# Kernel optimization log

Measured on AMD Instinct MI355X. Metric: run time of the kernel, lower is better.

## Reference

```python
import jax, jax.numpy as jnp
import numpy as np

B, N, F_ATOM, F_PATH = 32, 64, 82, 102
H, DK, HIDDEN, DEPTH = 8, 80, 256, 3
EPS = 1e-20


def setup_inputs() -> dict:
    key = jax.random.key(0)
    ks = jax.random.split(key, 12)
    s = lambda shape: 0.05
    inp = {
        "atom_input": jax.random.normal(ks[0], (B, N, F_ATOM), jnp.float32),
        "path_input": jax.random.normal(ks[1], (B, N, N, F_PATH), jnp.float32),
        # binary neighbor mask (path_mask); mask_neigh=True -> attn_mask = path_mask
        "path_mask": (jax.random.uniform(ks[2], (B, N, N)) < 0.25).astype(jnp.float32),
        "W_atom_i": jax.random.normal(ks[3], (F_ATOM, H * DK), jnp.float32) * 0.05,
        "W_attn_h": jax.random.normal(ks[4], (2 * DK + F_PATH, DK), jnp.float32) * 0.05,
        "b_attn_h": jax.random.normal(ks[5], (DK,), jnp.float32) * 0.05,
        "W_attn_o": jax.random.normal(ks[6], (DK, 1), jnp.float32) * 0.05,
        "b_attn_o": jax.random.normal(ks[7], (1,), jnp.float32) * 0.05,
        "W_msg_h": jax.random.normal(ks[8], (2 * DK + F_PATH, DK), jnp.float32) * 0.05,
        "b_msg_h": jax.random.normal(ks[9], (DK,), jnp.float32) * 0.05,
        "W_atom_o": jax.random.normal(ks[10], (F_ATOM + H * DK, HIDDEN), jnp.float32) * 0.05,
        "b_atom_o": jax.random.normal(ks[11], (HIDDEN,), jnp.float32) * 0.05,
    }
    return inp


def _forward(atom_input, path_input, path_mask,
             W_atom_i, W_attn_h, b_attn_h, W_attn_o, b_attn_o,
             W_msg_h, b_msg_h, W_atom_o, b_atom_o):
    # project atoms and split heads: [B,N,H*DK] -> [H*B, N, DK]
    atom_h0 = (atom_input @ W_atom_i).reshape(B, N, H, DK)
    atom_h0 = jnp.transpose(atom_h0, (2, 0, 1, 3)).reshape(H * B, N, DK)

    # tile path features / mask across heads (torch .repeat(n_heads,1,1,1))
    path_t = jnp.tile(path_input, (H, 1, 1, 1))          # [H*B, N, N, F_PATH]
    mask_t = jnp.tile(path_mask, (H, 1, 1))[..., None]    # [H*B, N, N, 1]

    atom_h = atom_h0
    for _ in range(DEPTH - 1):
        # pairwise expand + concat: [H*B, N, N, 2*DK + F_PATH]
        a1 = jnp.broadcast_to(atom_h[:, :, None, :], (H * B, N, N, DK))
        a2 = jnp.broadcast_to(atom_h[:, None, :, :], (H * B, N, N, DK))
        attn_input = jnp.concatenate([a1, a2, path_t], axis=3)

        # score MLP -> masked softmax over dim 2 (neighbors j)
        scores = jax.nn.leaky_relu(attn_input @ W_attn_h + b_attn_h, 0.2)
        scores = (scores @ W_attn_o + b_attn_o) * mask_t      # [H*B,N,N,1]
        max_s = jnp.max(scores, axis=2, keepdims=True)
        exp_s = jnp.exp(scores - max_s) * mask_t
        probs = exp_s / (jnp.sum(exp_s, axis=2, keepdims=True) + EPS) * mask_t

        # weighted message sum + residual
        msg = jnp.sum(probs * attn_input, axis=2)             # [H*B, N, 2DK+F_PATH]
        atom_h = jax.nn.relu(msg @ W_msg_h + b_msg_h + atom_h0)

    # merge heads back: [H*B,N,DK] -> [B,N,H*DK] -> [B*N, H*DK]
    atom_h = atom_h.reshape(H, B, N, DK)
    atom_h = jnp.transpose(atom_h, (1, 2, 0, 3)).reshape(B * N, H * DK)

    atom_2d = atom_input.reshape(B * N, F_ATOM)
    out = jnp.concatenate([atom_2d, atom_h], axis=1)
    return jax.nn.relu(out @ W_atom_o + b_atom_o)             # [B*N, HIDDEN]


def reference(atom_input, path_input, path_mask,
              W_atom_i, W_attn_h, b_attn_h, W_attn_o, b_attn_o,
              W_msg_h, b_msg_h, W_atom_o, b_atom_o):
    return _forward(atom_input, path_input, path_mask,
                    W_atom_i, W_attn_h, b_attn_h, W_attn_o, b_attn_o,
                    W_msg_h, b_msg_h, W_atom_o, b_atom_o)
```

## Files before the change

### kernel.cpp

```cpp
#include <hip/hip_runtime.h>
#include <hip/hip_bf16.h>

typedef __hip_bfloat16 bf16;
typedef _Float16 half2v __attribute__((ext_vector_type(2)));
typedef _Float16 half8  __attribute__((ext_vector_type(8)));
typedef float  float4v __attribute__((ext_vector_type(4)));
typedef unsigned uint4v __attribute__((ext_vector_type(4)));
typedef short  short8 __attribute__((ext_vector_type(8)));
typedef float  f32x4  __attribute__((ext_vector_type(4)));


__device__ inline float bflo(unsigned w) { return __uint_as_float(w << 16); }
__device__ inline float bfhi(unsigned w) { return __uint_as_float(w & 0xFFFF0000u); }
__device__ inline unsigned pack2bf(float x, float y) {
    bf16 a = (bf16)x, c = (bf16)y;
    unsigned short ua = *(unsigned short*)&a, uc = *(unsigned short*)&c;
    return (unsigned)ua | ((unsigned)uc << 16);
}
__device__ inline unsigned pack2h(float x, float y) {
    _Float16 a = (_Float16)x, c = (_Float16)y;
    unsigned short ua = *(unsigned short*)&a, uc = *(unsigned short*)&c;
    return (unsigned)ua | ((unsigned)uc << 16);
}
__device__ inline half2v ash2(unsigned u) { return __builtin_bit_cast(half2v, u); }
__device__ inline unsigned asu2(half2v h) { return __builtin_bit_cast(unsigned, h); }

__device__ inline float fdot2acc(half2v a, half2v b, float s) {
#if __has_builtin(__builtin_amdgcn_fdot2)
    return __builtin_amdgcn_fdot2(a, b, s, false);
#else
    return s + (float)a.x * (float)b.x + (float)a.y * (float)b.y;
#endif
}

__global__ __launch_bounds__(256) void prep_kernel(
    const float* __restrict__ W_atom_i, const float* __restrict__ W_attn_h,
    const float* __restrict__ b_attn_h, const float* __restrict__ W_msg_h,
    const float* __restrict__ W_atom_o,
    bf16* __restrict__ WTg, bf16* __restrict__ WTu, bf16* __restrict__ WTa,
    _Float16* __restrict__ WTo, float* __restrict__ buvam)
{
    int tid0 = blockIdx.x * 256 + threadIdx.x;
    int NT = gridDim.x * 256;
    for (int t = tid0; t < 2 * 80 * 128; t += NT) {
        int z = t / 10240, rem = t - z * 10240;
        int n = rem >> 7, k = rem & 127;
        const float* src = z ? W_msg_h : W_attn_h;
        WTg[t] = (bf16)((k < 102) ? src[(160 + k) * 80 + n] : 0.f);
    }
    for (int t = tid0; t < 4 * 80 * 96; t += NT) {
        int z = t / 7680, rem = t - z * 7680;
        int n = rem / 96, k = rem - n * 96;
        const float* src = (z < 2) ? W_attn_h : W_msg_h;
        WTu[t] = (bf16)((k < 80) ? src[((z & 1) * 80 + k) * 80 + n] : 0.f);
    }
    for (int t = tid0; t < 8 * 80 * 96; t += NT) {
        int h = t / 7680, rem = t - h * 7680;
        int n = rem / 96, k = rem - n * 96;
        WTa[t] = (bf16)((k < 82) ? W_atom_i[k * 640 + h * 80 + n] : 0.f);
    }
    for (int t = tid0; t < 256 * 736; t += NT) {
        int n = t / 736, f = t - n * 736;
        WTo[t] = (_Float16)((f < 722) ? W_atom_o[(size_t)f * 256 + n] : 0.f);
    }
    for (int t = tid0; t < 320; t += NT)
        buvam[t] = (t < 80) ? b_attn_h[t] : 0.f;
}

__global__ __launch_bounds__(320) void atom_proj_mfma(
    const float* __restrict__ atom, const bf16* __restrict__ WTa,
    float* __restrict__ ah0)
{
    __shared__ bf16 Als[64 * 104];
    int t = threadIdx.x;
    int rowBase = blockIdx.x * 64;
    int h = blockIdx.y;
    int wave = t >> 6, lane = t & 63, ln = lane & 15, quad = lane >> 4;

    const short* Wp = (const short*)(WTa + (size_t)h * 80 * 96);
    short8 bfrag[3];
    #pragma unroll
    for (int kc = 0; kc < 3; kc++)
        bfrag[kc] = *(const short8*)(Wp + (wave * 16 + ln) * 96 + kc * 32 + quad * 8);

    size_t abase = (size_t)rowBase * 82;
    for (int e = t; e < 5248; e += 320) {
        int r = e / 82, c = e - r * 82;
        Als[r * 104 + c] = (bf16)atom[abase + e];
    }
    for (int e = t; e < 896; e += 320) {
        int r = e / 14, c = 82 + (e - r * 14);
        Als[r * 104 + c] = (bf16)0.f;
    }
    __syncthreads();

    const short* Ap = (const short*)Als;
    int nc = wave * 16 + ln;
    #pragma unroll
    for (int rt = 0; rt < 4; rt++) {
        f32x4 acc = (f32x4){0.f, 0.f, 0.f, 0.f};
        #pragma unroll
        for (int kc = 0; kc < 3; kc++) {
            short8 af = *(const short8*)(Ap + (rt * 16 + ln) * 104 + kc * 32 + quad * 8);
            acc = __builtin_amdgcn_mfma_f32_16x16x32_bf16(af, bfrag[kc], acc, 0, 0, 0);
        }
        #pragma unroll
        for (int r = 0; r < 4; r++) {
            int row = rowBase + rt * 16 + quad * 4 + r;
            int b = row >> 6, i = row & 63;
            ah0[(((size_t)(h * 32 + b)) * 64 + i) * 80 + nc] = acc[r];
        }
    }
}

__global__ __launch_bounds__(320) void path_gemm_mfma(
    const float* __restrict__ A,
    const bf16* __restrict__ WTg,
    _Float16* __restrict__ P2h, bf16* __restrict__ PM3)
{
    __shared__ bf16 Als[64 * 136];

    int t = threadIdx.x;
    int bx = blockIdx.x;
    size_t abase = (size_t)bx * 6528;

    int wave = t >> 6, lane = t & 63;
    int ln = lane & 15, quad = lane >> 4;

    const short* Wp = (const short*)WTg;
    short8 bfrag[2][4];
    #pragma unroll
    for (int z = 0; z < 2; z++)
        #pragma unroll
        for (int kc = 0; kc < 4; kc++)
            bfrag[z][kc] = *(const short8*)(
                Wp + (size_t)(z * 80 + wave * 16 + ln) * 128 + kc * 32 + quad * 8);

    for (int e = t; e < 6528; e += 320) {
        int r = e / 102, c = e - r * 102;
        Als[r * 136 + c] = (bf16)A[abase + e];
    }
    for (int e = t; e < 2176; e += 320) {
        int r = e / 34, c = 102 + (e - r * 34);
        Als[r * 136 + c] = (bf16)0.f;
    }
    __syncthreads();

    const short* Ap = (const short*)Als;
    int nc = wave * 16 + ln;

    #pragma unroll
    for (int rt = 0; rt < 4; rt++) {
        f32x4 acc0 = (f32x4){0.f, 0.f, 0.f, 0.f};
        f32x4 acc1 = (f32x4){0.f, 0.f, 0.f, 0.f};
        #pragma unroll
        for (int kc = 0; kc < 4; kc++) {
            short8 af = *(const short8*)(
                Ap + (rt * 16 + ln) * 136 + kc * 32 + quad * 8);
            acc0 = __builtin_amdgcn_mfma_f32_16x16x32_bf16(af, bfrag[0][kc], acc0, 0, 0, 0);
            acc1 = __builtin_amdgcn_mfma_f32_16x16x32_bf16(af, bfrag[1][kc], acc1, 0, 0, 0);
        }
        #pragma unroll
        for (int r = 0; r < 4; r++) {
            int m = rt * 16 + quad * 4 + r;
            size_t row = (size_t)bx * 64 + m;
            P2h[row * 80 + nc] = (_Float16)acc0[r];
            PM3[row * 80 + nc] = (bf16)acc1[r];
        }
    }
}

__global__ __launch_bounds__(320) void uvam_gemm_mfma(
    const float* __restrict__ A,
    const bf16* __restrict__ WTu,
    const float* __restrict__ buvam,
    unsigned* __restrict__ Ug, unsigned* __restrict__ Vg,
    unsigned* __restrict__ A1g, unsigned* __restrict__ AMg)
{
    __shared__ float Bounce[64 * 84];
    bf16* Als = (bf16*)Bounce;

    int t = threadIdx.x;
    int hb = blockIdx.x, z = blockIdx.y;
    int wave = t >> 6, lane = t & 63;
    int ln = lane & 15, quad = lane >> 4;

    const short* Wp = (const short*)(WTu + (size_t)z * 80 * 96);
    short8 bfrag[3];
    #pragma unroll
    for (int kc = 0; kc < 3; kc++)
        bfrag[kc] = *(const short8*)(Wp + (wave * 16 + ln) * 96 + kc * 32 + quad * 8);

    size_t abase = (size_t)hb * 64 * 80;
    for (int e = t; e < 5120; e += 320) {
        int r = e / 80, c = e - r * 80;
        Als[r * 104 + c] = (bf16)A[abase + e];
    }
    for (int e = t; e < 1024; e += 320) {
        int r = e >> 4, c = 80 + (e & 15);
        Als[r * 104 + c] = (bf16)0.f;
    }
    __syncthreads();

    const short* Ap = (const short*)Als;
    f32x4 acc[4];
    #pragma unroll
    for (int rt = 0; rt < 4; rt++) {
        acc[rt] = (f32x4){0.f, 0.f, 0.f, 0.f};
        #pragma unroll
        for (int kc = 0; kc < 3; kc++) {
            short8 af = *(const short8*)(Ap + (rt * 16 + ln) * 104 + kc * 32 + quad * 8);
            acc[rt] = __builtin_amdgcn_mfma_f32_16x16x32_bf16(af, bfrag[kc], acc[rt], 0, 0, 0);
        }
    }
    __syncthreads();

    float bv = buvam[z * 80 + wave * 16 + ln];
    #pragma unroll
    for (int rt = 0; rt < 4; rt++)
        #pragma unroll
        for (int r = 0; r < 4; r++) {
            int m = rt * 16 + quad * 4 + r;
            Bounce[m * 84 + wave * 16 + ln] = acc[rt][r] + bv;
        }
    __syncthreads();

    unsigned* o = (z == 0) ? Ug : (z == 1) ? Vg : (z == 2) ? A1g : AMg;
    bool f16 = z < 2;
    size_t obase = (size_t)hb * 2560;
    for (int e = t; e < 2560; e += 320) {
        int j = e / 40, kp = e - j * 40;
        float x0 = Bounce[j * 84 + 2 * kp], x1 = Bounce[j * 84 + 2 * kp + 1];
        o[obase + e] = f16 ? pack2h(x0, x1) : pack2bf(x0, x1);
    }
}

__global__ __launch_bounds__(256, 5) void attn_layer_kernel(
    const unsigned* __restrict__ Ug,
    const unsigned* __restrict__ Vg,
    const unsigned* __restrict__ A1g,
    const unsigned* __restrict__ AMg,
    const _Float16* __restrict__ P2h,
    const bf16* __restrict__ PM3,
    const float* __restrict__ mask,
    const float* __restrict__ w_attn_o, const float* __restrict__ b_attn_o,
    const float* __restrict__ b_msg_h,
    const float* __restrict__ ah0, float* __restrict__ ah_next)
{
    __shared__ unsigned VBu[64 * 41];
    __shared__ unsigned Uu[8 * 40];
    __shared__ unsigned A1u[8 * 40];
    __shared__ unsigned wo2[40];
    __shared__ float bm[80];
    __shared__ float PS[4][2][64];

    int x = blockIdx.x;
    int hb = x & 255, it = x >> 8;
    int b = hb & 31;
    int i0 = it * 8;
    int t = threadIdx.x;
    int wave = t >> 6, lane = t & 63;
    int iA = i0 + wave * 2;
    size_t gbase = (size_t)hb * 2560;

    const uint4v* prow0 = (const uint4v*)(P2h + ((size_t)(b * 64 + iA) * 64 + lane) * 80);
    const uint4v* prow1 = (const uint4v*)(P2h + ((size_t)(b * 64 + iA + 1) * 64 + lane) * 80);
    uint4v p0a[5], p1a[5];
    #pragma unroll
    for (int u = 0; u < 5; u++) { p0a[u] = prow0[u]; p1a[u] = prow1[u]; }

    for (int e = t; e < 2560; e += 256) {
        int j = e / 40, w = e - j * 40;
        VBu[j * 41 + w] = Vg[gbase + e];
    }
    for (int e = t; e < 320; e += 256) {
        int iq = e / 40, kp = e - iq * 40;
        Uu[e]  = Ug[gbase + (size_t)(i0 + iq) * 40 + kp];
        A1u[e] = A1g[gbase + (size_t)(i0 + iq) * 40 + kp];
    }
    if (t < 40) wo2[t] = pack2h(w_attn_o[2 * t], w_attn_o[2 * t + 1]);
    if (t < 80) bm[t] = b_msg_h[t];
    __syncthreads();

    float b0 = b_attn_o[0];
    int iq0 = wave * 2, iq1 = wave * 2 + 1;
    const half2v c06 = { (_Float16)0.6f, (_Float16)0.6f };
    const half2v c04 = { (_Float16)0.4f, (_Float16)0.4f };

    float s0 = 0.f, s1 = 0.f;
    {
        const unsigned* pu0 = (const unsigned*)p0a;
        const unsigned* pu1 = (const unsigned*)p1a;
        #pragma unroll
        for (int kp = 0; kp < 20; kp++) {
            half2v v2 = ash2(VBu[lane * 41 + kp]);
            half2v w2 = ash2(wo2[kp]);
            half2v x0 = ash2(Uu[iq0 * 40 + kp]) + v2 + ash2(pu0[kp]);
            half2v a0 = ash2(asu2(x0) & 0x7FFF7FFFu);
            s0 = fdot2acc(x0 * c06 + a0 * c04, w2, s0);
            half2v x1 = ash2(Uu[iq1 * 40 + kp]) + v2 + ash2(pu1[kp]);
            half2v a1 = ash2(asu2(x1) & 0x7FFF7FFFu);
            s1 = fdot2acc(x1 * c06 + a1 * c04, w2, s1);
        }
    }
    {
        uint4v p0b[5], p1b[5];
        #pragma unroll
        for (int u = 0; u < 5; u++) { p0b[u] = prow0[5 + u]; p1b[u] = prow1[5 + u]; }
        const unsigned* pu0 = (const unsigned*)p0b;
        const unsigned* pu1 = (const unsigned*)p1b;
        #pragma unroll
        for (int kp = 0; kp < 20; kp++) {
            half2v v2 = ash2(VBu[lane * 41 + 20 + kp]);
            half2v w2 = ash2(wo2[20 + kp]);
            half2v x0 = ash2(Uu[iq0 * 40 + 20 + kp]) + v2 + ash2(pu0[kp]);
            half2v a0 = ash2(asu2(x0) & 0x7FFF7FFFu);
            s0 = fdot2acc(x0 * c06 + a0 * c04, w2, s0);
            half2v x1 = ash2(Uu[iq1 * 40 + 20 + kp]) + v2 + ash2(pu1[kp]);
            half2v a1 = ash2(asu2(x1) & 0x7FFF7FFFu);
            s1 = fdot2acc(x1 * c06 + a1 * c04, w2, s1);
        }
    }

    float sp[2];
    #pragma unroll
    for (int q = 0; q < 2; q++) {
        float s = q ? s1 : s0;
        float mj = mask[(size_t)b * 4096 + (size_t)(iA + q) * 64 + lane];
        float sc = (s + b0) * mj;
        float m = sc;
        #pragma unroll
        for (int off = 1; off < 64; off <<= 1) m = fmaxf(m, __shfl_xor(m, off, 64));
        float e = expf(sc - m) * mj;
        float d = e;
        #pragma unroll
        for (int off = 1; off < 64; off <<= 1) d += __shfl_xor(d, off, 64);
        float p = e / (d + 1e-20f) * mj;
        PS[wave][q][lane] = p;
        float spv = p;
        #pragma unroll
        for (int off = 1; off < 64; off <<= 1) spv += __shfl_xor(spv, off, 64);
        sp[q] = spv;
    }

    if (lane < 40) {
        const unsigned* pm0 = (const unsigned*)(PM3 + ((size_t)(b * 64 + iA) * 64) * 80);
        const unsigned* pm1 = pm0 + 2560;
        const unsigned* amp = AMg + gbase;
        float a00 = 0.f, a01 = 0.f, a10 = 0.f, a11 = 0.f;
        #pragma unroll 8
        for (int j = 0; j < 64; j++) {
            unsigned u0 = pm0[j * 40 + lane];
            unsigned u1 = pm1[j * 40 + lane];
            unsigned aw = amp[j * 40 + lane];
            float am0 = bflo(aw), am1 = bfhi(aw);
            float p0 = PS[wave][0][j];
            float p1 = PS[wave][1][j];
            a00 += p0 * (bflo(u0) + am0);
            a01 += p0 * (bfhi(u0) + am1);
            a10 += p1 * (bflo(u1) + am0);
            a11 += p1 * (bfhi(u1) + am1);
        }

        int k0 = 2 * lane, k1 = 2 * lane + 1;
        #pragma unroll
        for (int q = 0; q < 2; q++) {
            int i = iA + q;
            int iq = wave * 2 + q;
            unsigned aw1 = A1u[iq * 40 + lane];
            size_t orow = ((size_t)hb * 64 + i) * 80;
            float mlo = (q == 0) ? a00 : a10;
            float mhi = (q == 0) ? a01 : a11;
            float pre0 = sp[q] * bflo(aw1) + mlo + bm[k0] + ah0[orow + k0];
            float pre1 = sp[q] * bfhi(aw1) + mhi + bm[k1] + ah0[orow + k1];
            ah_next[orow + k0] = pre0 > 0.f ? pre0 : 0.f;
            ah_next[orow + k1] = pre1 > 0.f ? pre1 : 0.f;
        }
    }
}

__global__ __launch_bounds__(256) void merge_kernel(
    const float* __restrict__ atom, const float* __restrict__ ah,
    _Float16* __restrict__ X)
{
    int r0 = blockIdx.x * 8;
    int t = threadIdx.x;
    for (int e = t; e < 8 * 736; e += 256) {
        int r = e / 736, f = e - r * 736;
        int row = r0 + r;
        float v;
        if (f < 82) {
            v = atom[(size_t)row * 82 + f];
        } else if (f < 722) {
            int q = f - 82, h = q / 80, k = q - h * 80;
            int b = row >> 6, i = row & 63;
            v = ah[(((size_t)(h * 32 + b)) * 64 + i) * 80 + k];
        } else {
            v = 0.f;
        }
        X[(size_t)row * 736 + f] = (_Float16)v;
    }
}

__global__ __launch_bounds__(256) void out_gemm_mfma(
    const _Float16* __restrict__ X, const _Float16* __restrict__ WTo,
    const float* __restrict__ bo, float* __restrict__ out)
{
    __shared__ _Float16 Als[16 * 744];
    int bx = blockIdx.x, by = blockIdx.y;
    int t = threadIdx.x;
    int wave = t >> 6, lane = t & 63, ln = lane & 15, quad = lane >> 4;

    {
        const unsigned* src = (const unsigned*)(X + (size_t)bx * 16 * 736);
        for (int e = t; e < 16 * 368; e += 256) {
            int r = e / 368, u = e - r * 368;
            *(unsigned*)(Als + r * 744 + u * 2) = src[r * 368 + u];
        }
    }
    __syncthreads();

    int nbase = by * 128 + wave * 32;
    f32x4 acc0 = (f32x4){0.f, 0.f, 0.f, 0.f};
    f32x4 acc1 = (f32x4){0.f, 0.f, 0.f, 0.f};
    const _Float16* Bp0 = WTo + (size_t)(nbase + ln) * 736 + quad * 8;
    const _Float16* Bp1 = WTo + (size_t)(nbase + 16 + ln) * 736 + quad * 8;

    #pragma unroll
    for (int kc = 0; kc < 23; kc++) {
        half8 af = *(const half8*)(Als + ln * 744 + kc * 32 + quad * 8);
        half8 b0 = *(const half8*)(Bp0 + kc * 32);
        half8 b1 = *(const half8*)(Bp1 + kc * 32);
        acc0 = __builtin_amdgcn_mfma_f32_16x16x32_f16(af, b0, acc0, 0, 0, 0);
        acc1 = __builtin_amdgcn_mfma_f32_16x16x32_f16(af, b1, acc1, 0, 0, 0);
    }

    #pragma unroll
    for (int f = 0; f < 2; f++) {
        int c = nbase + f * 16 + ln;
        float bias = bo[c];
        f32x4 a = f ? acc1 : acc0;
        #pragma unroll
        for (int r = 0; r < 4; r++) {
            int m = quad * 4 + r;
            float v = a[r] + bias;
            out[(size_t)(bx * 16 + m) * 256 + c] = v > 0.f ? v : 0.f;
        }
    }
}

extern "C" void kernel_launch(void* const* d_in, const int* in_sizes, int n_in,
                              void* d_out, int out_size, void* d_ws, size_t ws_size,
                              hipStream_t stream)
{
    const float* atom_input = (const float*)d_in[0];
    const float* path_input = (const float*)d_in[1];
    const float* path_mask  = (const float*)d_in[2];
    const float* W_atom_i   = (const float*)d_in[3];
    const float* W_attn_h   = (const float*)d_in[4];
    const float* b_attn_h   = (const float*)d_in[5];
    const float* W_attn_o   = (const float*)d_in[6];
    const float* b_attn_o   = (const float*)d_in[7];
    const float* W_msg_h    = (const float*)d_in[8];
    const float* b_msg_h    = (const float*)d_in[9];
    const float* W_atom_o   = (const float*)d_in[10];
    const float* b_atom_o   = (const float*)d_in[11];
    float* out = (float*)d_out;

    char* ws = (char*)d_ws;
    float*     ah0  = (float*)ws;     ws += (size_t)16384 * 80 * 4;
    float*     ah1  = (float*)ws;     ws += (size_t)16384 * 80 * 4;
    _Float16*  P2h  = (_Float16*)ws;  ws += (size_t)131072 * 80 * 2;
    bf16*      PM3  = (bf16*)ws;      ws += (size_t)131072 * 80 * 2;
    unsigned*  Ug   = (unsigned*)ws;  ws += (size_t)256 * 2560 * 4;
    unsigned*  Vg   = (unsigned*)ws;  ws += (size_t)256 * 2560 * 4;
    unsigned*  A1g  = (unsigned*)ws;  ws += (size_t)256 * 2560 * 4;
    unsigned*  AMg  = (unsigned*)ws;  ws += (size_t)256 * 2560 * 4;
    _Float16*  X    = (_Float16*)ws;  ws += (size_t)2048 * 736 * 2;
    bf16*      WTg  = (bf16*)ws;      ws += (size_t)2 * 80 * 128 * 2;
    bf16*      WTu  = (bf16*)ws;      ws += (size_t)4 * 80 * 96 * 2;
    bf16*      WTa  = (bf16*)ws;      ws += (size_t)8 * 80 * 96 * 2;
    _Float16*  WTo  = (_Float16*)ws;  ws += (size_t)256 * 736 * 2;
    float*     buvam= (float*)ws;     ws += (size_t)4 * 80 * 4;

    prep_kernel<<<256, 256, 0, stream>>>(W_atom_i, W_attn_h, b_attn_h, W_msg_h,
                                         W_atom_o, WTg, WTu, WTa, WTo, buvam);

    atom_proj_mfma<<<dim3(32, 8), 320, 0, stream>>>(atom_input, WTa, ah0);

    path_gemm_mfma<<<2048, 320, 0, stream>>>(path_input, WTg, P2h, PM3);

    const float* cur = ah0;
    float* nxt[2] = { ah1, ah1 };
    for (int layer = 0; layer < 2; layer++) {
        uvam_gemm_mfma<<<dim3(256, 4), 320, 0, stream>>>(
            cur, WTu, buvam, Ug, Vg, A1g, AMg);

        attn_layer_kernel<<<2048, 256, 0, stream>>>(
            Ug, Vg, A1g, AMg, P2h, PM3, path_mask, W_attn_o, b_attn_o, b_msg_h,
            ah0, nxt[layer]);
        cur = nxt[layer];
    }

    merge_kernel<<<256, 256, 0, stream>>>(atom_input, cur, X);
    out_gemm_mfma<<<dim3(128, 2), 256, 0, stream>>>(X, WTo, b_atom_o, out);
}
```

Before: 258.9 us.

## Store path projection in lane-interleaved layout and vectorize fp32 input loads

The path GEMM now writes the fp16 P2 projection in a transposed layout where each 16-byte chunk group is laid out contiguously across the 64 neighbor lanes. The attention kernel's per-lane uint4 loads are then coalesced instead of strided by 160 bytes. The output is staged through shared memory, which adds two barriers to the path GEMM. The input staging loops in three GEMM kernels also switch from scalar fp32 loads to float4 loads.

```diff
diff --git a/kernel.cpp b/kernel.cpp
--- a/kernel.cpp
+++ b/kernel.cpp
@@ -83,10 +83,18 @@
     for (int kc = 0; kc < 3; kc++)
         bfrag[kc] = *(const short8*)(Wp + (wave * 16 + ln) * 96 + kc * 32 + quad * 8);
 
-    size_t abase = (size_t)rowBase * 82;
-    for (int e = t; e < 5248; e += 320) {
-        int r = e / 82, c = e - r * 82;
-        Als[r * 104 + c] = (bf16)atom[abase + e];
+    {
+        const float4v* A4 = (const float4v*)(atom + (size_t)rowBase * 82);
+        for (int e4 = t; e4 < 1312; e4 += 320) {
+            float4v v = A4[e4];
+            int idx = e4 * 4;
+            #pragma unroll
+            for (int q = 0; q < 4; q++) {
+                int ii = idx + q;
+                int r = ii / 82, c = ii - r * 82;
+                Als[r * 104 + c] = (bf16)v[q];
+            }
+        }
     }
     for (int e = t; e < 896; e += 320) {
         int r = e / 14, c = 82 + (e - r * 14);
@@ -116,13 +124,12 @@
 __global__ __launch_bounds__(320) void path_gemm_mfma(
     const float* __restrict__ A,
     const bf16* __restrict__ WTg,
-    _Float16* __restrict__ P2h, bf16* __restrict__ PM3)
+    uint4v* __restrict__ PT4, bf16* __restrict__ PM3)
 {
     __shared__ bf16 Als[64 * 136];
 
     int t = threadIdx.x;
     int bx = blockIdx.x;
-    size_t abase = (size_t)bx * 6528;
 
     int wave = t >> 6, lane = t & 63;
     int ln = lane & 15, quad = lane >> 4;
@@ -136,9 +143,18 @@
             bfrag[z][kc] = *(const short8*)(
                 Wp + (size_t)(z * 80 + wave * 16 + ln) * 128 + kc * 32 + quad * 8);
 
-    for (int e = t; e < 6528; e += 320) {
-        int r = e / 102, c = e - r * 102;
-        Als[r * 136 + c] = (bf16)A[abase + e];
+    {
+        const float4v* A4 = (const float4v*)(A + (size_t)bx * 6528);
+        for (int e4 = t; e4 < 1632; e4 += 320) {
+            float4v v = A4[e4];
+            int idx = e4 * 4;
+            #pragma unroll
+            for (int q = 0; q < 4; q++) {
+                int ii = idx + q;
+                int r = ii / 102, c = ii - r * 102;
+                Als[r * 136 + c] = (bf16)v[q];
+            }
+        }
     }
     for (int e = t; e < 2176; e += 320) {
         int r = e / 34, c = 102 + (e - r * 34);
@@ -149,24 +165,45 @@
     const short* Ap = (const short*)Als;
     int nc = wave * 16 + ln;
 
+    f32x4 acc0[4], acc1[4];
     #pragma unroll
     for (int rt = 0; rt < 4; rt++) {
-        f32x4 acc0 = (f32x4){0.f, 0.f, 0.f, 0.f};
-        f32x4 acc1 = (f32x4){0.f, 0.f, 0.f, 0.f};
+        acc0[rt] = (f32x4){0.f, 0.f, 0.f, 0.f};
+        acc1[rt] = (f32x4){0.f, 0.f, 0.f, 0.f};
         #pragma unroll
         for (int kc = 0; kc < 4; kc++) {
             short8 af = *(const short8*)(
                 Ap + (rt * 16 + ln) * 136 + kc * 32 + quad * 8);
-            acc0 = __builtin_amdgcn_mfma_f32_16x16x32_bf16(af, bfrag[0][kc], acc0, 0, 0, 0);
-            acc1 = __builtin_amdgcn_mfma_f32_16x16x32_bf16(af, bfrag[1][kc], acc1, 0, 0, 0);
-        }
+            acc0[rt] = __builtin_amdgcn_mfma_f32_16x16x32_bf16(af, bfrag[0][kc], acc0[rt], 0, 0, 0);
+            acc1[rt] = __builtin_amdgcn_mfma_f32_16x16x32_bf16(af, bfrag[1][kc], acc1[rt], 0, 0, 0);
+        }
+    }
+
+    #pragma unroll
+    for (int rt = 0; rt < 4; rt++)
         #pragma unroll
         for (int r = 0; r < 4; r++) {
             int m = rt * 16 + quad * 4 + r;
-            size_t row = (size_t)bx * 64 + m;
-            P2h[row * 80 + nc] = (_Float16)acc0[r];
-            PM3[row * 80 + nc] = (bf16)acc1[r];
-        }
+            PM3[(size_t)bx * 5120 + m * 80 + nc] = (bf16)acc1[rt][r];
+        }
+
+    __syncthreads();
+    _Float16* Cb = (_Float16*)Als;
+    #pragma unroll
+    for (int rt = 0; rt < 4; rt++)
+        #pragma unroll
+        for (int r = 0; r < 4; r++) {
+            int m = rt * 16 + quad * 4 + r;
+            Cb[m * 84 + nc] = (_Float16)acc0[rt][r];
+        }
+    __syncthreads();
+
+    uint4v* dst = PT4 + (size_t)bx * 640;
+    for (int e = t; e < 640; e += 320) {
+        int g = e >> 6, j = e & 63;
+        const unsigned* src = (const unsigned*)(Cb + j * 84 + g * 8);
+        uint4v v = { src[0], src[1], src[2], src[3] };
+        dst[(size_t)g * 64 + j] = v;
     }
 }
 
@@ -191,10 +228,16 @@
     for (int kc = 0; kc < 3; kc++)
         bfrag[kc] = *(const short8*)(Wp + (wave * 16 + ln) * 96 + kc * 32 + quad * 8);
 
-    size_t abase = (size_t)hb * 64 * 80;
-    for (int e = t; e < 5120; e += 320) {
-        int r = e / 80, c = e - r * 80;
-        Als[r * 104 + c] = (bf16)A[abase + e];
+    {
+        const float4v* A4 = (const float4v*)(A + (size_t)hb * 5120);
+        for (int e4 = t; e4 < 1280; e4 += 320) {
+            float4v v = A4[e4];
+            int idx = e4 * 4;
+            int r = idx / 80, c = idx - r * 80;
+            #pragma unroll
+            for (int q = 0; q < 4; q++)
+                Als[r * 104 + c + q] = (bf16)v[q];
+        }
     }
     for (int e = t; e < 1024; e += 320) {
         int r = e >> 4, c = 80 + (e & 15);
@@ -240,7 +283,7 @@
     const unsigned* __restrict__ Vg,
     const unsigned* __restrict__ A1g,
     const unsigned* __restrict__ AMg,
-    const _Float16* __restrict__ P2h,
+    const uint4v* __restrict__ PT4,
     const bf16* __restrict__ PM3,
     const float* __restrict__ mask,
     const float* __restrict__ w_attn_o, const float* __restrict__ b_attn_o,
@@ -263,11 +306,11 @@
     int iA = i0 + wave * 2;
     size_t gbase = (size_t)hb * 2560;
 
-    const uint4v* prow0 = (const uint4v*)(P2h + ((size_t)(b * 64 + iA) * 64 + lane) * 80);
-    const uint4v* prow1 = (const uint4v*)(P2h + ((size_t)(b * 64 + iA + 1) * 64 + lane) * 80);
+    const uint4v* prow0 = PT4 + (size_t)(b * 64 + iA) * 640 + lane;
+    const uint4v* prow1 = prow0 + 640;
     uint4v p0a[5], p1a[5];
     #pragma unroll
-    for (int u = 0; u < 5; u++) { p0a[u] = prow0[u]; p1a[u] = prow1[u]; }
+    for (int u = 0; u < 5; u++) { p0a[u] = prow0[u * 64]; p1a[u] = prow1[u * 64]; }
 
     for (int e = t; e < 2560; e += 256) {
         int j = e / 40, w = e - j * 40;
@@ -306,7 +349,10 @@
     {
         uint4v p0b[5], p1b[5];
         #pragma unroll
-        for (int u = 0; u < 5; u++) { p0b[u] = prow0[5 + u]; p1b[u] = prow1[5 + u]; }
+        for (int u = 0; u < 5; u++) {
+            p0b[u] = prow0[(5 + u) * 64];
+            p1b[u] = prow1[(5 + u) * 64];
+        }
         const unsigned* pu0 = (const unsigned*)p0b;
         const unsigned* pu1 = (const unsigned*)p1b;
         #pragma unroll
@@ -470,7 +516,7 @@
     char* ws = (char*)d_ws;
     float*     ah0  = (float*)ws;     ws += (size_t)16384 * 80 * 4;
     float*     ah1  = (float*)ws;     ws += (size_t)16384 * 80 * 4;
-    _Float16*  P2h  = (_Float16*)ws;  ws += (size_t)131072 * 80 * 2;
+    uint4v*    PT4  = (uint4v*)ws;    ws += (size_t)2048 * 640 * 16;
     bf16*      PM3  = (bf16*)ws;      ws += (size_t)131072 * 80 * 2;
     unsigned*  Ug   = (unsigned*)ws;  ws += (size_t)256 * 2560 * 4;
     unsigned*  Vg   = (unsigned*)ws;  ws += (size_t)256 * 2560 * 4;
@@ -488,7 +534,7 @@
 
     atom_proj_mfma<<<dim3(32, 8), 320, 0, stream>>>(atom_input, WTa, ah0);
 
-    path_gemm_mfma<<<2048, 320, 0, stream>>>(path_input, WTg, P2h, PM3);
+    path_gemm_mfma<<<2048, 320, 0, stream>>>(path_input, WTg, PT4, PM3);
 
     const float* cur = ah0;
     float* nxt[2] = { ah1, ah1 };
@@ -497,7 +543,7 @@
             cur, WTu, buvam, Ug, Vg, A1g, AMg);
 
         attn_layer_kernel<<<2048, 256, 0, stream>>>(
-            Ug, Vg, A1g, AMg, P2h, PM3, path_mask, W_attn_o, b_attn_o, b_msg_h,
+            Ug, Vg, A1g, AMg, PT4, PM3, path_mask, W_attn_o, b_attn_o, b_msg_h,
             ah0, nxt[layer]);
         cur = nxt[layer];
     }
```

Result: faster. 229.2 us (-11.5%).
